# Kernel optimization log

Hardware: AMD Instinct MI355X
Metric: run time of the kernel (lower is better)

The kernel has to match this reference:

```python
import jax, jax.numpy as jnp
import numpy as np

BATCH, LENGTH = 4, 512
D_MODEL, D_STATE, EXPAND = 128, 256, 2
D_INNER = EXPAND * D_MODEL  # 256 (== D_STATE, required by the original broadcasting)


def setup_inputs() -> dict:
    key = jax.random.key(0)
    ks = jax.random.split(key, 8)
    x = jax.random.normal(ks[0], (BATCH, LENGTH, D_MODEL), jnp.float32)
    # bias-free Dense kernels, fan-in scaled; W_delta and A kept small so
    # exp(delta*A)^L stays numerically tame over L=512 steps.
    W_in = jax.random.normal(ks[1], (D_MODEL, 2 * D_INNER), jnp.float32) / np.float32(np.sqrt(D_MODEL))
    W_delta = jax.random.normal(ks[2], (D_INNER, D_INNER), jnp.float32) * np.float32(0.005)
    W_B = jax.random.normal(ks[3], (D_INNER, D_STATE), jnp.float32) / np.float32(np.sqrt(D_INNER))
    W_C = jax.random.normal(ks[4], (D_INNER, D_INNER), jnp.float32) / np.float32(np.sqrt(D_INNER))
    W_out = jax.random.normal(ks[5], (D_INNER, D_MODEL), jnp.float32) / np.float32(np.sqrt(D_INNER))
    A = jax.random.normal(ks[6], (D_INNER, D_STATE), jnp.float32) * np.float32(0.02)
    D = jnp.ones((D_INNER,), jnp.float32)  # unused by the original scan, kept for faithfulness
    return dict(x=x, W_in=W_in, W_delta=W_delta, W_B=W_B, W_C=W_C, W_out=W_out, A=A, D=D)


def reference(x, W_in, W_delta, W_B, W_C, W_out, A, D):
    # in_proj + split
    x_proj = x @ W_in                      # (b, l, 2*d_inner)
    xs, z = jnp.split(x_proj, 2, axis=-1)  # each (b, l, d_inner)
    delta = xs @ W_delta                   # (b, l, d_inner)
    Bv = xs @ W_B                          # (b, l, d_state)
    Cv = xs @ W_C                          # (b, l, d_inner)

    # discretized transition/input, exactly as the original einsums
    deltaA = jnp.exp(jnp.einsum('bld,dn->bldn', delta, A))   # (b, l, d_inner, d_state)
    deltaB = jnp.einsum('bld,bln->bldn', delta, Bv)          # (b, l, d_inner, d_state)

    def step(state, inp):
        dA_i, dB_i, x_i, C_i = inp
        # state: (b, d_inner, d_state); x broadcast over the middle axis as in tf.expand_dims(x,1)
        state = dA_i * state + dB_i * x_i[:, None, :]
        y = jnp.einsum('bdn,bn->bd', state, C_i)
        return state, y

    init = jnp.zeros((x.shape[0], D_INNER, D_STATE), xs.dtype)
    inps = (
        jnp.moveaxis(deltaA, 1, 0),  # (l, b, d, n)
        jnp.moveaxis(deltaB, 1, 0),
        jnp.moveaxis(xs, 1, 0),      # (l, b, d)
        jnp.moveaxis(Cv, 1, 0),
    )
    _, ys = jax.lax.scan(step, init, inps)   # ys: (l, b, d_inner)
    y = jnp.moveaxis(ys, 0, 1)               # (b, l, d_inner)

    y = y * jax.nn.silu(z)
    return y @ W_out                          # (b, l, d_model)
```

## Files before the change

### kernel.cpp

```cpp
#include <hip/hip_runtime.h>
#include <hip/hip_bf16.h>


#define MROWS 2048
#define DM 128
#define DI 256
#define DS 256
#define LLEN 512
#define LC 64
#define NC 8

#define LOG2E 1.44269504088896340736f

typedef short bf16x8 __attribute__((ext_vector_type(8)));
typedef float f32x4  __attribute__((ext_vector_type(4)));

__device__ __forceinline__ short f2bf(float f) {
    union { float f; unsigned u; } v; v.f = f;
    unsigned r = v.u + 0x7FFFu + ((v.u >> 16) & 1u);
    return (short)(r >> 16);
}

#define TEXP(c1, c2, c3, dl) fmaf(fmaf(fmaf((c3), (dl), (c2)), (dl), (c1)), (dl), 1.f)

__device__ __forceinline__ void tconv(float (*tile)[33],
                                      const float* __restrict__ src,
                                      short* __restrict__ dst,
                                      int Ms, int Ns, int ti, int tj, int tid)
{
    const int r = tid >> 5, c = tid & 31;
#pragma unroll
    for (int i = 0; i < 4; ++i)
        tile[r + 8 * i][c] = src[(size_t)(ti * 32 + r + 8 * i) * Ns + tj * 32 + c];
    __syncthreads();
#pragma unroll
    for (int i = 0; i < 4; ++i)
        dst[(size_t)(tj * 32 + r + 8 * i) * Ms + ti * 32 + c] = f2bf(tile[c][r + 8 * i]);
}

__global__ __launch_bounds__(256) void k_prep(
    const float* __restrict__ x, const float* __restrict__ W_in,
    const float* __restrict__ Wd, const float* __restrict__ Wb,
    const float* __restrict__ Wc, const float* __restrict__ W_out,
    short* __restrict__ x_bf, short* __restrict__ W_inT,
    short* __restrict__ WdbcT, short* __restrict__ W_outT)
{
    __shared__ float tile[32][33];
    const int bid = blockIdx.x;
    const int t = threadIdx.x;
    if (bid < 128) {
        const size_t base = (size_t)bid * 2048 + (size_t)t * 8;
        float4 f0 = *(const float4*)(x + base);
        float4 f1 = *(const float4*)(x + base + 4);
        bf16x8 o;
        o[0] = f2bf(f0.x); o[1] = f2bf(f0.y); o[2] = f2bf(f0.z); o[3] = f2bf(f0.w);
        o[4] = f2bf(f1.x); o[5] = f2bf(f1.y); o[6] = f2bf(f1.z); o[7] = f2bf(f1.w);
        *(bf16x8*)(x_bf + base) = o;
    } else if (bid < 192) {
        const int bb = bid - 128;
        tconv(tile, W_in, W_inT, 128, 512, bb & 3, bb >> 2, t);
    } else if (bid < 256) {
        const int bb = bid - 192;
        tconv(tile, Wd, WdbcT, 256, 256, bb & 7, bb >> 3, t);
    } else if (bid < 320) {
        const int bb = bid - 256;
        tconv(tile, Wb, WdbcT + (size_t)256 * 256, 256, 256, bb & 7, bb >> 3, t);
    } else if (bid < 384) {
        const int bb = bid - 320;
        tconv(tile, Wc, WdbcT + (size_t)512 * 256, 256, 256, bb & 7, bb >> 3, t);
    } else {
        const int bb = bid - 384;
        tconv(tile, W_out, W_outT, 256, 128, bb & 7, bb >> 3, t);
    }
}

#define BKK 64
#define LP  72

__device__ __forceinline__ void mfma_core64(
    const short* __restrict__ Abf, int lda,
    const short* __restrict__ BbfT, int ldb,
    int K, int r0, int n0,
    short (*As)[LP], short (*Bs)[LP], f32x4 acc[4])
{
    const int tid  = threadIdx.x;
    const int w    = tid >> 6, lane = tid & 63;
    const int srow = tid >> 2, sseg = tid & 3;
    const int frow = lane & 15, fk = (lane >> 4) << 3;

    for (int k0 = 0; k0 < K; k0 += BKK) {
        const short* ag = Abf  + (size_t)(r0 + srow) * lda + k0 + sseg * 16;
        const short* bg = BbfT + (size_t)(n0 + srow) * ldb + k0 + sseg * 16;
        bf16x8 a0 = *(const bf16x8*)ag;
        bf16x8 a1 = *(const bf16x8*)(ag + 8);
        bf16x8 b0 = *(const bf16x8*)bg;
        bf16x8 b1 = *(const bf16x8*)(bg + 8);
        __syncthreads();
        *(bf16x8*)&As[srow][sseg * 16]     = a0;
        *(bf16x8*)&As[srow][sseg * 16 + 8] = a1;
        *(bf16x8*)&Bs[srow][sseg * 16]     = b0;
        *(bf16x8*)&Bs[srow][sseg * 16 + 8] = b1;
        __syncthreads();
#pragma unroll
        for (int kk = 0; kk < BKK; kk += 32) {
            bf16x8 af = *(const bf16x8*)&As[w * 16 + frow][kk + fk];
#pragma unroll
            for (int ct = 0; ct < 4; ++ct) {
                bf16x8 bfr = *(const bf16x8*)&Bs[ct * 16 + frow][kk + fk];
                acc[ct] = __builtin_amdgcn_mfma_f32_16x16x32_bf16(af, bfr, acc[ct], 0, 0, 0);
            }
        }
    }
}

__global__ __launch_bounds__(256) void k_proj_mfma(
    const short* __restrict__ x_bf, const short* __restrict__ W_inT,
    float* __restrict__ xs, short* __restrict__ xs_bf, float* __restrict__ sz)
{
    __shared__ short As[64][LP], Bs[64][LP];
    f32x4 acc[4] = {};
    const int r0 = blockIdx.y * 64, n0 = blockIdx.x * 64;
    mfma_core64(x_bf, DM, W_inT, DM, DM, r0, n0, As, Bs, acc);
    const int lane = threadIdx.x & 63, w = threadIdx.x >> 6;
    const int rr = r0 + w * 16 + (lane >> 4) * 4;
    const int c0 = n0 + (lane & 15);
#pragma unroll
    for (int ct = 0; ct < 4; ++ct) {
        const int c = c0 + ct * 16;
#pragma unroll
        for (int rg = 0; rg < 4; ++rg) {
            const float v = acc[ct][rg];
            const int r = rr + rg;
            if (c < DI) {
                xs[(size_t)r * DI + c]    = v;
                xs_bf[(size_t)r * DI + c] = f2bf(v);
            } else {
                sz[(size_t)r * DI + (c - DI)] = v / (1.f + __expf(-v));
            }
        }
    }
}

__global__ __launch_bounds__(256) void k_dbc_mfma(
    const short* __restrict__ xs_bf, const short* __restrict__ WdbcT,
    const float* __restrict__ xs,
    float* __restrict__ dlt, float* __restrict__ u, float* __restrict__ cvv)
{
    __shared__ short As[64][LP], Bs[64][LP];
    f32x4 acc[4] = {};
    const int r0 = blockIdx.y * 64, n0 = blockIdx.x * 64;
    mfma_core64(xs_bf, DI, WdbcT, DI, DI, r0, n0, As, Bs, acc);
    const int lane = threadIdx.x & 63, w = threadIdx.x >> 6;
    const int rr = r0 + w * 16 + (lane >> 4) * 4;
    const int wsel = n0 >> 8;
    const int nb = n0 & 255;
#pragma unroll
    for (int ct = 0; ct < 4; ++ct) {
        const int c = nb + ct * 16 + (lane & 15);
#pragma unroll
        for (int rg = 0; rg < 4; ++rg) {
            const float v = acc[ct][rg];
            const size_t idx = (size_t)(rr + rg) * DI + c;
            if (wsel == 0)      dlt[idx] = v;
            else if (wsel == 1) u[idx]   = v * xs[idx];
            else                cvv[idx] = v;
        }
    }
}

__global__ __launch_bounds__(256) void k_scan1(
    const float* __restrict__ dlt, const float* __restrict__ u,
    const float* __restrict__ A,
    float* __restrict__ tc, float* __restrict__ dsum)
{
    const int lane = threadIdx.x & 63;
    const int w    = threadIdx.x >> 6;
    const int blk  = blockIdx.x;
    const int b  = blk & 3;
    const int c  = (blk >> 2) & 7;
    const int d0 = ((blk >> 5) * 4 + w) * 4;

    __shared__ float dls[4][4][LC];

    const size_t base = (size_t)b * LLEN * DI + (size_t)c * LC * DI;

    float4 dv = *(const float4*)(dlt + base + (size_t)lane * DI + d0);
    dls[w][0][lane] = dv.x;
    dls[w][1][lane] = dv.y;
    dls[w][2][lane] = dv.z;
    dls[w][3][lane] = dv.w;
    float dsv[4] = { dv.x, dv.y, dv.z, dv.w };
#pragma unroll
    for (int dd = 0; dd < 4; ++dd) {
#pragma unroll
        for (int off = 32; off > 0; off >>= 1)
            dsv[dd] += __shfl_xor(dsv[dd], off);
    }
    __syncthreads();

    float4 c1[4], c2[4], c3[4];
#pragma unroll
    for (int dd = 0; dd < 4; ++dd) {
        float4 a = *(const float4*)(A + (size_t)(d0 + dd) * DS + lane * 4);
        c1[dd] = a;
        c2[dd] = make_float4(0.5f * a.x * a.x, 0.5f * a.y * a.y,
                             0.5f * a.z * a.z, 0.5f * a.w * a.w);
        c3[dd] = make_float4(c2[dd].x * a.x * (1.f / 3.f), c2[dd].y * a.y * (1.f / 3.f),
                             c2[dd].z * a.z * (1.f / 3.f), c2[dd].w * a.w * (1.f / 3.f));
    }

    const float4* up = (const float4*)(u + base) + lane;
    float4 s[4] = {};
    float4 ub[2][4];

#define S1_PRE(NXT, G1)                                                       \
    {                                                                         \
        _Pragma("unroll")                                                     \
        for (int i = 0; i < 4; ++i)                                           \
            ub[NXT][i] = up[(size_t)((G1) * 4 + i) * 64];                     \
    }

#define S1_STEP4(CUR, G)                                                      \
    {                                                                         \
        _Pragma("unroll")                                                     \
        for (int i0 = 0; i0 < 4; ++i0) {                                      \
            const int l = (G) * 4 + i0;                                       \
            const float4 uv = ub[CUR][i0];                                    \
            _Pragma("unroll")                                                 \
            for (int dd = 0; dd < 4; ++dd) {                                  \
                const float dl = dls[w][dd][l];                               \
                s[dd].x = fmaf(TEXP(c1[dd].x, c2[dd].x, c3[dd].x, dl), s[dd].x, dl * uv.x); \
                s[dd].y = fmaf(TEXP(c1[dd].y, c2[dd].y, c3[dd].y, dl), s[dd].y, dl * uv.y); \
                s[dd].z = fmaf(TEXP(c1[dd].z, c2[dd].z, c3[dd].z, dl), s[dd].z, dl * uv.z); \
                s[dd].w = fmaf(TEXP(c1[dd].w, c2[dd].w, c3[dd].w, dl), s[dd].w, dl * uv.w); \
            }                                                                 \
        }                                                                     \
    }

    S1_PRE(0, 0)
    for (int g2 = 0; g2 < 8; ++g2) {
        S1_PRE(1, g2 * 2 + 1)
        S1_STEP4(0, g2 * 2)
        if (g2 < 7) S1_PRE(0, g2 * 2 + 2)
        S1_STEP4(1, g2 * 2 + 1)
    }
#undef S1_PRE
#undef S1_STEP4

    const size_t rbb = ((size_t)(b * 256 + d0)) * NC + c;
#pragma unroll
    for (int dd = 0; dd < 4; ++dd) {
        *(float4*)(tc + (rbb + (size_t)dd * NC) * 256 + lane * 4) = s[dd];
        if (lane == 0) dsum[rbb + dd * NC] = dsv[dd];
    }
}

__global__ __launch_bounds__(256) void k_scan2(
    const float* __restrict__ A, float* __restrict__ tc,
    const float* __restrict__ dsum)
{
    const int lane = threadIdx.x & 63;
    const int w    = threadIdx.x >> 6;
    const int blk  = blockIdx.x;
    const int b = blk & 3;
    const int d = (blk >> 2) * 4 + w;

    float4 a4 = *(const float4*)(A + (size_t)d * DS + lane * 4);
    a4.x *= LOG2E; a4.y *= LOG2E; a4.z *= LOG2E; a4.w *= LOG2E;

    const size_t rb = ((size_t)(b * 256 + d)) * NC;
    float4 s = make_float4(0.f, 0.f, 0.f, 0.f);
#pragma unroll
    for (int c = 0; c < NC; ++c) {
        float* p = tc + (rb + c) * 256 + lane * 4;
        float4 T = *(const float4*)p;
        float  Dc = dsum[rb + c];
        *(float4*)p = s;
        s.x = exp2f(a4.x * Dc) * s.x + T.x;
        s.y = exp2f(a4.y * Dc) * s.y + T.y;
        s.z = exp2f(a4.z * Dc) * s.z + T.z;
        s.w = exp2f(a4.w * Dc) * s.w + T.w;
    }
}

__global__ __launch_bounds__(256) void k_scan3(
    const float* __restrict__ dlt, const float* __restrict__ u,
    const float* __restrict__ cv, const float* __restrict__ A,
    const float* __restrict__ tc, float* __restrict__ y)
{
    const int lane = threadIdx.x & 63;
    const int w    = threadIdx.x >> 6;
    const int blk  = blockIdx.x;
    const int b  = blk & 3;
    const int c  = (blk >> 2) & 7;
    const int d0 = ((blk >> 5) * 4 + w) * 4;

    __shared__ float dls[4][4][LC];
    __shared__ float T[4][LC][33];

    const size_t base = (size_t)b * LLEN * DI + (size_t)c * LC * DI;

    float4 dv = *(const float4*)(dlt + base + (size_t)lane * DI + d0);
    dls[w][0][lane] = dv.x;
    dls[w][1][lane] = dv.y;
    dls[w][2][lane] = dv.z;
    dls[w][3][lane] = dv.w;
    __syncthreads();

    float4 c1[4], c2[4], c3[4];
#pragma unroll
    for (int dd = 0; dd < 4; ++dd) {
        float4 a = *(const float4*)(A + (size_t)(d0 + dd) * DS + lane * 4);
        c1[dd] = a;
        c2[dd] = make_float4(0.5f * a.x * a.x, 0.5f * a.y * a.y,
                             0.5f * a.z * a.z, 0.5f * a.w * a.w);
        c3[dd] = make_float4(c2[dd].x * a.x * (1.f / 3.f), c2[dd].y * a.y * (1.f / 3.f),
                             c2[dd].z * a.z * (1.f / 3.f), c2[dd].w * a.w * (1.f / 3.f));
    }

    const float4* up = (const float4*)(u + base) + lane;
    const float4* cp = (const float4*)(cv + base) + lane;
    float* yb = y + base;

    const size_t rbb = ((size_t)(b * 256 + d0)) * NC + c;
    float4 s[4];
#pragma unroll
    for (int dd = 0; dd < 4; ++dd)
        s[dd] = *(const float4*)(tc + (rbb + (size_t)dd * NC) * 256 + lane * 4);

    float4 ub[2][4], cb[2][4];
    float  p[4][8];

#define S3_PRE(NXT, G1)                                                       \
    {                                                                         \
        _Pragma("unroll")                                                     \
        for (int i = 0; i < 4; ++i) {                                         \
            ub[NXT][i] = up[(size_t)((G1) * 4 + i) * 64];                     \
            cb[NXT][i] = cp[(size_t)((G1) * 4 + i) * 64];                     \
        }                                                                     \
    }

#define S3_STEP4(CUR, G, PBASE)                                               \
    {                                                                         \
        _Pragma("unroll")                                                     \
        for (int i0 = 0; i0 < 4; ++i0) {                                      \
            const int l = (G) * 4 + i0;                                       \
            const float4 uv = ub[CUR][i0];                                    \
            const float4 cV = cb[CUR][i0];                                    \
            _Pragma("unroll")                                                 \
            for (int dd = 0; dd < 4; ++dd) {                                  \
                const float dl = dls[w][dd][l];                               \
                s[dd].x = fmaf(TEXP(c1[dd].x, c2[dd].x, c3[dd].x, dl), s[dd].x, dl * uv.x); \
                s[dd].y = fmaf(TEXP(c1[dd].y, c2[dd].y, c3[dd].y, dl), s[dd].y, dl * uv.y); \
                s[dd].z = fmaf(TEXP(c1[dd].z, c2[dd].z, c3[dd].z, dl), s[dd].z, dl * uv.z); \
                s[dd].w = fmaf(TEXP(c1[dd].w, c2[dd].w, c3[dd].w, dl), s[dd].w, dl * uv.w); \
                p[dd][(PBASE) + i0] =                                         \
                    fmaf(s[dd].w, cV.w, fmaf(s[dd].z, cV.z,                   \
                         fmaf(s[dd].y, cV.y, s[dd].x * cV.x)));               \
            }                                                                 \
        }                                                                     \
    }

#define S3_FLUSH(GODD)                                                        \
    {                                                                         \
        float* tr = &T[w][lane][0];                                           \
        _Pragma("unroll")                                                     \
        for (int dd = 0; dd < 4; ++dd) {                                      \
            *(float4*)(tr + dd * 8)     = make_float4(p[dd][0], p[dd][1], p[dd][2], p[dd][3]); \
            *(float4*)(tr + dd * 8 + 4) = make_float4(p[dd][4], p[dd][5], p[dd][6], p[dd][7]); \
        }                                                                     \
        const int cc = lane & 31, seg = lane >> 5;                            \
        float sm = 0.f;                                                       \
        _Pragma("unroll")                                                     \
        for (int r = 0; r < 32; ++r)                                          \
            sm += T[w][seg * 32 + r][cc];                                     \
        sm += __shfl_xor(sm, 32);                                             \
        if (lane < 32)                                                        \
            yb[(size_t)(((GODD) - 1) * 4 + (cc & 7)) * DI + d0 + (cc >> 3)] = sm; \
    }

    S3_PRE(0, 0)
    for (int g2 = 0; g2 < 8; ++g2) {
        S3_PRE(1, g2 * 2 + 1)
        S3_STEP4(0, g2 * 2, 0)
        if (g2 < 7) S3_PRE(0, g2 * 2 + 2)
        S3_STEP4(1, g2 * 2 + 1, 4)
        S3_FLUSH(g2 * 2 + 1)
        if ((g2 & 1) == 1) __syncthreads();
    }
#undef S3_PRE
#undef S3_STEP4
#undef S3_FLUSH
}

__global__ __launch_bounds__(256) void k_out_mfma(
    const float* __restrict__ y, const float* __restrict__ szp,
    const short* __restrict__ W_outT, float* __restrict__ out)
{
    __shared__ short As[64][LP], Bs[64][LP];
    f32x4 acc[4] = {};
    const int tid  = threadIdx.x;
    const int w    = tid >> 6, lane = tid & 63;
    const int srow = tid >> 2, sseg = tid & 3;
    const int frow = lane & 15, fk = (lane >> 4) << 3;
    const int r0 = blockIdx.y * 64, n0 = blockIdx.x * 64;

    for (int k0 = 0; k0 < DI; k0 += BKK) {
        const size_t aoff = (size_t)(r0 + srow) * DI + k0 + sseg * 16;
        float4 y0 = *(const float4*)(y + aoff);
        float4 y1 = *(const float4*)(y + aoff + 4);
        float4 y2 = *(const float4*)(y + aoff + 8);
        float4 y3 = *(const float4*)(y + aoff + 12);
        float4 s0 = *(const float4*)(szp + aoff);
        float4 s1 = *(const float4*)(szp + aoff + 4);
        float4 s2 = *(const float4*)(szp + aoff + 8);
        float4 s3 = *(const float4*)(szp + aoff + 12);
        const short* bg = W_outT + (size_t)(n0 + srow) * DI + k0 + sseg * 16;
        bf16x8 b0 = *(const bf16x8*)bg;
        bf16x8 b1 = *(const bf16x8*)(bg + 8);
        bf16x8 a0, a1;
        a0[0] = f2bf(y0.x * s0.x); a0[1] = f2bf(y0.y * s0.y);
        a0[2] = f2bf(y0.z * s0.z); a0[3] = f2bf(y0.w * s0.w);
        a0[4] = f2bf(y1.x * s1.x); a0[5] = f2bf(y1.y * s1.y);
        a0[6] = f2bf(y1.z * s1.z); a0[7] = f2bf(y1.w * s1.w);
        a1[0] = f2bf(y2.x * s2.x); a1[1] = f2bf(y2.y * s2.y);
        a1[2] = f2bf(y2.z * s2.z); a1[3] = f2bf(y2.w * s2.w);
        a1[4] = f2bf(y3.x * s3.x); a1[5] = f2bf(y3.y * s3.y);
        a1[6] = f2bf(y3.z * s3.z); a1[7] = f2bf(y3.w * s3.w);
        __syncthreads();
        *(bf16x8*)&As[srow][sseg * 16]     = a0;
        *(bf16x8*)&As[srow][sseg * 16 + 8] = a1;
        *(bf16x8*)&Bs[srow][sseg * 16]     = b0;
        *(bf16x8*)&Bs[srow][sseg * 16 + 8] = b1;
        __syncthreads();
#pragma unroll
        for (int kk = 0; kk < BKK; kk += 32) {
            bf16x8 af = *(const bf16x8*)&As[w * 16 + frow][kk + fk];
#pragma unroll
            for (int ct = 0; ct < 4; ++ct) {
                bf16x8 bfr = *(const bf16x8*)&Bs[ct * 16 + frow][kk + fk];
                acc[ct] = __builtin_amdgcn_mfma_f32_16x16x32_bf16(af, bfr, acc[ct], 0, 0, 0);
            }
        }
    }

    const int rr = r0 + w * 16 + (lane >> 4) * 4;
    const int c0 = n0 + (lane & 15);
#pragma unroll
    for (int ct = 0; ct < 4; ++ct) {
        const int c = c0 + ct * 16;
#pragma unroll
        for (int rg = 0; rg < 4; ++rg)
            out[(size_t)(rr + rg) * DM + c] = acc[ct][rg];
    }
}

extern "C" void kernel_launch(void* const* d_in, const int* in_sizes, int n_in,
                              void* d_out, int out_size, void* d_ws, size_t ws_size,
                              hipStream_t stream)
{
    const float* x       = (const float*)d_in[0];
    const float* W_in    = (const float*)d_in[1];
    const float* W_delta = (const float*)d_in[2];
    const float* W_B     = (const float*)d_in[3];
    const float* W_C     = (const float*)d_in[4];
    const float* W_out   = (const float*)d_in[5];
    const float* A       = (const float*)d_in[6];

    float* out = (float*)d_out;
    float* ws  = (float*)d_ws;

    const size_t S = (size_t)MROWS * DI;
    float* xs  = ws;
    float* sz  = ws + S;
    float* dlt = ws + 2 * S;
    float* u   = ws + 3 * S;
    float* cv  = ws + 4 * S;
    float* yv  = ws + 5 * S;
    float* tc  = ws + 6 * S;
    float* dsm = ws + 6 * S + (size_t)1024 * NC * 256;

    short* bfb    = (short*)(dsm + 1024 * NC);
    short* x_bf   = bfb;
    short* xs_bf  = x_bf + (size_t)MROWS * DM;
    short* W_inT  = xs_bf + (size_t)MROWS * DI;
    short* WdbcT  = W_inT + (size_t)512 * DM;
    short* W_outT = WdbcT + (size_t)768 * DI;

    k_prep     <<<dim3(416), 256, 0, stream>>>(x, W_in, W_delta, W_B, W_C, W_out,
                                               x_bf, W_inT, WdbcT, W_outT);
    k_proj_mfma<<<dim3(8, 32), 256, 0, stream>>>(x_bf, W_inT, xs, xs_bf, sz);
    k_dbc_mfma <<<dim3(12, 32), 256, 0, stream>>>(xs_bf, WdbcT, xs, dlt, u, cv);
    k_scan1    <<<dim3(512), 256, 0, stream>>>(dlt, u, A, tc, dsm);
    k_scan2    <<<dim3(256), 256, 0, stream>>>(A, tc, dsm);
    k_scan3    <<<dim3(512), 256, 0, stream>>>(dlt, u, cv, A, tc, yv);
    k_out_mfma <<<dim3(2, 32), 256, 0, stream>>>(yv, sz, W_outT, out);
}
```

Measured before the change: 76.54 us.

## Fuse prep into projection GEMM, halve scan chunk length, simplify scan loops

Folds the bf16 conversion and weight-transpose prep kernel into the input projection kernel, which now converts x and W_in on the fly and uses extra blocks to transpose the other weights. This removes one launch and the x_bf/W_inT round trip. The scan chunk length drops from 64 to 32 with 16 chunks, doubling the scan1/scan3 grids for more parallelism at the cost of a longer inter-chunk scan2, which now preloads its chunk values into registers. The scan loops drop their double-buffered prefetch and some __syncthreads, and add launch-bounds occupancy hints.

Result: no change. 77.77 us (+1.6%).

```diff
diff --git a/kernel.cpp b/kernel.cpp
--- a/kernel.cpp
+++ b/kernel.cpp
@@ -7,8 +7,8 @@
 #define DI 256
 #define DS 256
 #define LLEN 512
-#define LC 64
-#define NC 8
+#define LC 32
+#define NC 16
 
 #define LOG2E 1.44269504088896340736f
 
@@ -38,39 +38,84 @@
         dst[(size_t)(tj * 32 + r + 8 * i) * Ms + ti * 32 + c] = f2bf(tile[c][r + 8 * i]);
 }
 
-__global__ __launch_bounds__(256) void k_prep(
+__global__ __launch_bounds__(256) void k_proj_mfma(
     const float* __restrict__ x, const float* __restrict__ W_in,
     const float* __restrict__ Wd, const float* __restrict__ Wb,
     const float* __restrict__ Wc, const float* __restrict__ W_out,
-    short* __restrict__ x_bf, short* __restrict__ W_inT,
+    float* __restrict__ xs, short* __restrict__ xs_bf, float* __restrict__ sz,
     short* __restrict__ WdbcT, short* __restrict__ W_outT)
 {
-    __shared__ float tile[32][33];
-    const int bid = blockIdx.x;
     const int t = threadIdx.x;
-    if (bid < 128) {
-        const size_t base = (size_t)bid * 2048 + (size_t)t * 8;
-        float4 f0 = *(const float4*)(x + base);
-        float4 f1 = *(const float4*)(x + base + 4);
-        bf16x8 o;
-        o[0] = f2bf(f0.x); o[1] = f2bf(f0.y); o[2] = f2bf(f0.z); o[3] = f2bf(f0.w);
-        o[4] = f2bf(f1.x); o[5] = f2bf(f1.y); o[6] = f2bf(f1.z); o[7] = f2bf(f1.w);
-        *(bf16x8*)(x_bf + base) = o;
-    } else if (bid < 192) {
-        const int bb = bid - 128;
-        tconv(tile, W_in, W_inT, 128, 512, bb & 3, bb >> 2, t);
-    } else if (bid < 256) {
-        const int bb = bid - 192;
-        tconv(tile, Wd, WdbcT, 256, 256, bb & 7, bb >> 3, t);
-    } else if (bid < 320) {
-        const int bb = bid - 256;
-        tconv(tile, Wb, WdbcT + (size_t)256 * 256, 256, 256, bb & 7, bb >> 3, t);
-    } else if (bid < 384) {
-        const int bb = bid - 320;
-        tconv(tile, Wc, WdbcT + (size_t)512 * 256, 256, 256, bb & 7, bb >> 3, t);
-    } else {
-        const int bb = bid - 384;
-        tconv(tile, W_out, W_outT, 256, 128, bb & 7, bb >> 3, t);
+
+    if (blockIdx.x >= 8) {
+        __shared__ float tile[32][33];
+        const int uu = (blockIdx.x - 8) * 32 + blockIdx.y;
+        if (uu < 64)       tconv(tile, Wd,    WdbcT,                       256, 256, uu & 7,         uu >> 3,         t);
+        else if (uu < 128) tconv(tile, Wb,    WdbcT + (size_t)256 * 256,   256, 256, (uu - 64) & 7,  (uu - 64) >> 3,  t);
+        else if (uu < 192) tconv(tile, Wc,    WdbcT + (size_t)512 * 256,   256, 256, (uu - 128) & 7, (uu - 128) >> 3, t);
+        else if (uu < 224) tconv(tile, W_out, W_outT,                      256, 128, (uu - 192) & 7, (uu - 192) >> 3, t);
+        return;
+    }
+
+    __shared__ short As[64][136];
+    __shared__ short Bs[64][136];
+    f32x4 acc[4] = {};
+    const int w = t >> 6, lane = t & 63;
+    const int srow = t >> 2, sseg = t & 3;
+    const int frow = lane & 15, fk = (lane >> 4) << 3;
+    const int r0 = blockIdx.y * 64, n0 = blockIdx.x * 64;
+
+    {
+        const float* ap = x + (size_t)(r0 + srow) * DM + sseg * 32;
+        short tmp[32];
+#pragma unroll
+        for (int j = 0; j < 8; ++j) {
+            float4 f = *(const float4*)(ap + j * 4);
+            tmp[j * 4 + 0] = f2bf(f.x); tmp[j * 4 + 1] = f2bf(f.y);
+            tmp[j * 4 + 2] = f2bf(f.z); tmp[j * 4 + 3] = f2bf(f.w);
+        }
+#pragma unroll
+        for (int m = 0; m < 4; ++m)
+            *(bf16x8*)&As[srow][sseg * 32 + m * 8] = *(bf16x8*)&tmp[m * 8];
+    }
+    {
+#pragma unroll
+        for (int i = 0; i < 32; i += 2) {
+            const int k = sseg * 32 + i;
+            float f0 = W_in[(size_t)k * 512 + n0 + srow];
+            float f1 = W_in[(size_t)(k + 1) * 512 + n0 + srow];
+            unsigned pk = (unsigned short)f2bf(f0) | ((unsigned)(unsigned short)f2bf(f1) << 16);
+            *(unsigned*)&Bs[srow][k] = pk;
+        }
+    }
+    __syncthreads();
+
+#pragma unroll
+    for (int kk = 0; kk < 128; kk += 32) {
+        bf16x8 af = *(const bf16x8*)&As[w * 16 + frow][kk + fk];
+#pragma unroll
+        for (int ct = 0; ct < 4; ++ct) {
+            bf16x8 bfr = *(const bf16x8*)&Bs[ct * 16 + frow][kk + fk];
+            acc[ct] = __builtin_amdgcn_mfma_f32_16x16x32_bf16(af, bfr, acc[ct], 0, 0, 0);
+        }
+    }
+
+    const int rr = r0 + w * 16 + (lane >> 4) * 4;
+    const int c0 = n0 + (lane & 15);
+#pragma unroll
+    for (int ct = 0; ct < 4; ++ct) {
+        const int c = c0 + ct * 16;
+#pragma unroll
+        for (int rg = 0; rg < 4; ++rg) {
+            const float v = acc[ct][rg];
+            const int r = rr + rg;
+            if (c < DI) {
+                xs[(size_t)r * DI + c]    = v;
+                xs_bf[(size_t)r * DI + c] = f2bf(v);
+            } else {
+                sz[(size_t)r * DI + (c - DI)] = v / (1.f + __expf(-v));
+            }
+        }
     }
 }
 
@@ -113,34 +158,6 @@
     }
 }
 
-__global__ __launch_bounds__(256) void k_proj_mfma(
-    const short* __restrict__ x_bf, const short* __restrict__ W_inT,
-    float* __restrict__ xs, short* __restrict__ xs_bf, float* __restrict__ sz)
-{
-    __shared__ short As[64][LP], Bs[64][LP];
-    f32x4 acc[4] = {};
-    const int r0 = blockIdx.y * 64, n0 = blockIdx.x * 64;
-    mfma_core64(x_bf, DM, W_inT, DM, DM, r0, n0, As, Bs, acc);
-    const int lane = threadIdx.x & 63, w = threadIdx.x >> 6;
-    const int rr = r0 + w * 16 + (lane >> 4) * 4;
-    const int c0 = n0 + (lane & 15);
-#pragma unroll
-    for (int ct = 0; ct < 4; ++ct) {
-        const int c = c0 + ct * 16;
-#pragma unroll
-        for (int rg = 0; rg < 4; ++rg) {
-            const float v = acc[ct][rg];
-            const int r = rr + rg;
-            if (c < DI) {
-                xs[(size_t)r * DI + c]    = v;
-                xs_bf[(size_t)r * DI + c] = f2bf(v);
-            } else {
-                sz[(size_t)r * DI + (c - DI)] = v / (1.f + __expf(-v));
-            }
-        }
-    }
-}
-
 __global__ __launch_bounds__(256) void k_dbc_mfma(
     const short* __restrict__ xs_bf, const short* __restrict__ WdbcT,
     const float* __restrict__ xs,
@@ -168,7 +185,8 @@
     }
 }
 
-__global__ __launch_bounds__(256) void k_scan1(
+
+__global__ __launch_bounds__(256, 4) void k_scan1(
     const float* __restrict__ dlt, const float* __restrict__ u,
     const float* __restrict__ A,
     float* __restrict__ tc, float* __restrict__ dsum)
@@ -177,18 +195,21 @@
     const int w    = threadIdx.x >> 6;
     const int blk  = blockIdx.x;
     const int b  = blk & 3;
-    const int c  = (blk >> 2) & 7;
-    const int d0 = ((blk >> 5) * 4 + w) * 4;
+    const int c  = (blk >> 2) & 15;
+    const int d0 = ((blk >> 6) * 4 + w) * 4;
 
     __shared__ float dls[4][4][LC];
 
     const size_t base = (size_t)b * LLEN * DI + (size_t)c * LC * DI;
 
-    float4 dv = *(const float4*)(dlt + base + (size_t)lane * DI + d0);
-    dls[w][0][lane] = dv.x;
-    dls[w][1][lane] = dv.y;
-    dls[w][2][lane] = dv.z;
-    dls[w][3][lane] = dv.w;
+    float4 dv = make_float4(0.f, 0.f, 0.f, 0.f);
+    if (lane < LC) {
+        dv = *(const float4*)(dlt + base + (size_t)lane * DI + d0);
+        dls[w][0][lane] = dv.x;
+        dls[w][1][lane] = dv.y;
+        dls[w][2][lane] = dv.z;
+        dls[w][3][lane] = dv.w;
+    }
     float dsv[4] = { dv.x, dv.y, dv.z, dv.w };
 #pragma unroll
     for (int dd = 0; dd < 4; ++dd) {
@@ -196,7 +217,6 @@
         for (int off = 32; off > 0; off >>= 1)
             dsv[dd] += __shfl_xor(dsv[dd], off);
     }
-    __syncthreads();
 
     float4 c1[4], c2[4], c3[4];
 #pragma unroll
@@ -211,41 +231,25 @@
 
     const float4* up = (const float4*)(u + base) + lane;
     float4 s[4] = {};
-    float4 ub[2][4];
-
-#define S1_PRE(NXT, G1)                                                       \
-    {                                                                         \
-        _Pragma("unroll")                                                     \
-        for (int i = 0; i < 4; ++i)                                           \
-            ub[NXT][i] = up[(size_t)((G1) * 4 + i) * 64];                     \
-    }
-
-#define S1_STEP4(CUR, G)                                                      \
-    {                                                                         \
-        _Pragma("unroll")                                                     \
-        for (int i0 = 0; i0 < 4; ++i0) {                                      \
-            const int l = (G) * 4 + i0;                                       \
-            const float4 uv = ub[CUR][i0];                                    \
-            _Pragma("unroll")                                                 \
-            for (int dd = 0; dd < 4; ++dd) {                                  \
-                const float dl = dls[w][dd][l];                               \
-                s[dd].x = fmaf(TEXP(c1[dd].x, c2[dd].x, c3[dd].x, dl), s[dd].x, dl * uv.x); \
-                s[dd].y = fmaf(TEXP(c1[dd].y, c2[dd].y, c3[dd].y, dl), s[dd].y, dl * uv.y); \
-                s[dd].z = fmaf(TEXP(c1[dd].z, c2[dd].z, c3[dd].z, dl), s[dd].z, dl * uv.z); \
-                s[dd].w = fmaf(TEXP(c1[dd].w, c2[dd].w, c3[dd].w, dl), s[dd].w, dl * uv.w); \
-            }                                                                 \
-        }                                                                     \
-    }
-
-    S1_PRE(0, 0)
-    for (int g2 = 0; g2 < 8; ++g2) {
-        S1_PRE(1, g2 * 2 + 1)
-        S1_STEP4(0, g2 * 2)
-        if (g2 < 7) S1_PRE(0, g2 * 2 + 2)
-        S1_STEP4(1, g2 * 2 + 1)
-    }
-#undef S1_PRE
-#undef S1_STEP4
+
+    for (int g = 0; g < LC / 4; ++g) {
+        float4 uv[4];
+#pragma unroll
+        for (int i = 0; i < 4; ++i)
+            uv[i] = up[(size_t)(g * 4 + i) * 64];
+#pragma unroll
+        for (int i = 0; i < 4; ++i) {
+            const int l = g * 4 + i;
+#pragma unroll
+            for (int dd = 0; dd < 4; ++dd) {
+                const float dl = dls[w][dd][l];
+                s[dd].x = fmaf(TEXP(c1[dd].x, c2[dd].x, c3[dd].x, dl), s[dd].x, dl * uv[i].x);
+                s[dd].y = fmaf(TEXP(c1[dd].y, c2[dd].y, c3[dd].y, dl), s[dd].y, dl * uv[i].y);
+                s[dd].z = fmaf(TEXP(c1[dd].z, c2[dd].z, c3[dd].z, dl), s[dd].z, dl * uv[i].z);
+                s[dd].w = fmaf(TEXP(c1[dd].w, c2[dd].w, c3[dd].w, dl), s[dd].w, dl * uv[i].w);
+            }
+        }
+    }
 
     const size_t rbb = ((size_t)(b * 256 + d0)) * NC + c;
 #pragma unroll
@@ -269,21 +273,29 @@
     a4.x *= LOG2E; a4.y *= LOG2E; a4.z *= LOG2E; a4.w *= LOG2E;
 
     const size_t rb = ((size_t)(b * 256 + d)) * NC;
+    float4 T[NC];
+    float  Dc[NC];
+#pragma unroll
+    for (int c = 0; c < NC; ++c) {
+        T[c]  = *(const float4*)(tc + (rb + c) * 256 + lane * 4);
+        Dc[c] = dsum[rb + c];
+    }
     float4 s = make_float4(0.f, 0.f, 0.f, 0.f);
 #pragma unroll
     for (int c = 0; c < NC; ++c) {
-        float* p = tc + (rb + c) * 256 + lane * 4;
-        float4 T = *(const float4*)p;
-        float  Dc = dsum[rb + c];
-        *(float4*)p = s;
-        s.x = exp2f(a4.x * Dc) * s.x + T.x;
-        s.y = exp2f(a4.y * Dc) * s.y + T.y;
-        s.z = exp2f(a4.z * Dc) * s.z + T.z;
-        s.w = exp2f(a4.w * Dc) * s.w + T.w;
-    }
-}
-
-__global__ __launch_bounds__(256) void k_scan3(
+        float4 tmp = T[c];
+        T[c] = s;
+        s.x = exp2f(a4.x * Dc[c]) * s.x + tmp.x;
+        s.y = exp2f(a4.y * Dc[c]) * s.y + tmp.y;
+        s.z = exp2f(a4.z * Dc[c]) * s.z + tmp.z;
+        s.w = exp2f(a4.w * Dc[c]) * s.w + tmp.w;
+    }
+#pragma unroll
+    for (int c = 0; c < NC; ++c)
+        *(float4*)(tc + (rb + c) * 256 + lane * 4) = T[c];
+}
+
+__global__ __launch_bounds__(256, 4) void k_scan3(
     const float* __restrict__ dlt, const float* __restrict__ u,
     const float* __restrict__ cv, const float* __restrict__ A,
     const float* __restrict__ tc, float* __restrict__ y)
@@ -292,20 +304,21 @@
     const int w    = threadIdx.x >> 6;
     const int blk  = blockIdx.x;
     const int b  = blk & 3;
-    const int c  = (blk >> 2) & 7;
-    const int d0 = ((blk >> 5) * 4 + w) * 4;
+    const int c  = (blk >> 2) & 15;
+    const int d0 = ((blk >> 6) * 4 + w) * 4;
 
     __shared__ float dls[4][4][LC];
-    __shared__ float T[4][LC][33];
+    __shared__ float T[4][64][33];
 
     const size_t base = (size_t)b * LLEN * DI + (size_t)c * LC * DI;
 
-    float4 dv = *(const float4*)(dlt + base + (size_t)lane * DI + d0);
-    dls[w][0][lane] = dv.x;
-    dls[w][1][lane] = dv.y;
-    dls[w][2][lane] = dv.z;
-    dls[w][3][lane] = dv.w;
-    __syncthreads();
+    if (lane < LC) {
+        float4 dv = *(const float4*)(dlt + base + (size_t)lane * DI + d0);
+        dls[w][0][lane] = dv.x;
+        dls[w][1][lane] = dv.y;
+        dls[w][2][lane] = dv.z;
+        dls[w][3][lane] = dv.w;
+    }
 
     float4 c1[4], c2[4], c3[4];
 #pragma unroll
@@ -328,69 +341,41 @@
     for (int dd = 0; dd < 4; ++dd)
         s[dd] = *(const float4*)(tc + (rbb + (size_t)dd * NC) * 256 + lane * 4);
 
-    float4 ub[2][4], cb[2][4];
-    float  p[4][8];
-
-#define S3_PRE(NXT, G1)                                                       \
-    {                                                                         \
-        _Pragma("unroll")                                                     \
-        for (int i = 0; i < 4; ++i) {                                         \
-            ub[NXT][i] = up[(size_t)((G1) * 4 + i) * 64];                     \
-            cb[NXT][i] = cp[(size_t)((G1) * 4 + i) * 64];                     \
-        }                                                                     \
-    }
-
-#define S3_STEP4(CUR, G, PBASE)                                               \
-    {                                                                         \
-        _Pragma("unroll")                                                     \
-        for (int i0 = 0; i0 < 4; ++i0) {                                      \
-            const int l = (G) * 4 + i0;                                       \
-            const float4 uv = ub[CUR][i0];                                    \
-            const float4 cV = cb[CUR][i0];                                    \
-            _Pragma("unroll")                                                 \
-            for (int dd = 0; dd < 4; ++dd) {                                  \
-                const float dl = dls[w][dd][l];                               \
-                s[dd].x = fmaf(TEXP(c1[dd].x, c2[dd].x, c3[dd].x, dl), s[dd].x, dl * uv.x); \
-                s[dd].y = fmaf(TEXP(c1[dd].y, c2[dd].y, c3[dd].y, dl), s[dd].y, dl * uv.y); \
-                s[dd].z = fmaf(TEXP(c1[dd].z, c2[dd].z, c3[dd].z, dl), s[dd].z, dl * uv.z); \
-                s[dd].w = fmaf(TEXP(c1[dd].w, c2[dd].w, c3[dd].w, dl), s[dd].w, dl * uv.w); \
-                p[dd][(PBASE) + i0] =                                         \
-                    fmaf(s[dd].w, cV.w, fmaf(s[dd].z, cV.z,                   \
-                         fmaf(s[dd].y, cV.y, s[dd].x * cV.x)));               \
-            }                                                                 \
-        }                                                                     \
-    }
-
-#define S3_FLUSH(GODD)                                                        \
-    {                                                                         \
-        float* tr = &T[w][lane][0];                                           \
-        _Pragma("unroll")                                                     \
-        for (int dd = 0; dd < 4; ++dd) {                                      \
-            *(float4*)(tr + dd * 8)     = make_float4(p[dd][0], p[dd][1], p[dd][2], p[dd][3]); \
-            *(float4*)(tr + dd * 8 + 4) = make_float4(p[dd][4], p[dd][5], p[dd][6], p[dd][7]); \
-        }                                                                     \
-        const int cc = lane & 31, seg = lane >> 5;                            \
-        float sm = 0.f;                                                       \
-        _Pragma("unroll")                                                     \
-        for (int r = 0; r < 32; ++r)                                          \
-            sm += T[w][seg * 32 + r][cc];                                     \
-        sm += __shfl_xor(sm, 32);                                             \
-        if (lane < 32)                                                        \
-            yb[(size_t)(((GODD) - 1) * 4 + (cc & 7)) * DI + d0 + (cc >> 3)] = sm; \
-    }
-
-    S3_PRE(0, 0)
-    for (int g2 = 0; g2 < 8; ++g2) {
-        S3_PRE(1, g2 * 2 + 1)
-        S3_STEP4(0, g2 * 2, 0)
-        if (g2 < 7) S3_PRE(0, g2 * 2 + 2)
-        S3_STEP4(1, g2 * 2 + 1, 4)
-        S3_FLUSH(g2 * 2 + 1)
-        if ((g2 & 1) == 1) __syncthreads();
-    }
-#undef S3_PRE
-#undef S3_STEP4
-#undef S3_FLUSH
+    const int cc = lane & 31, seg = lane >> 5;
+
+    for (int g = 0; g < LC / 4; ++g) {
+        float4 uv[4], cV[4];
+#pragma unroll
+        for (int i = 0; i < 4; ++i) {
+            uv[i] = up[(size_t)(g * 4 + i) * 64];
+            cV[i] = cp[(size_t)(g * 4 + i) * 64];
+        }
+#pragma unroll
+        for (int i = 0; i < 4; ++i) {
+            const int l = g * 4 + i;
+            const int lc = l & 7;
+#pragma unroll
+            for (int dd = 0; dd < 4; ++dd) {
+                const float dl = dls[w][dd][l];
+                s[dd].x = fmaf(TEXP(c1[dd].x, c2[dd].x, c3[dd].x, dl), s[dd].x, dl * uv[i].x);
+                s[dd].y = fmaf(TEXP(c1[dd].y, c2[dd].y, c3[dd].y, dl), s[dd].y, dl * uv[i].y);
+                s[dd].z = fmaf(TEXP(c1[dd].z, c2[dd].z, c3[dd].z, dl), s[dd].z, dl * uv[i].z);
+                s[dd].w = fmaf(TEXP(c1[dd].w, c2[dd].w, c3[dd].w, dl), s[dd].w, dl * uv[i].w);
+                T[w][lane][dd * 8 + lc] =
+                    fmaf(s[dd].w, cV[i].w, fmaf(s[dd].z, cV[i].z,
+                         fmaf(s[dd].y, cV[i].y, s[dd].x * cV[i].x)));
+            }
+        }
+        if (g & 1) {
+            float sm = 0.f;
+#pragma unroll
+            for (int r = 0; r < 32; ++r)
+                sm += T[w][seg * 32 + r][cc];
+            sm += __shfl_xor(sm, 32);
+            if (lane < 32)
+                yb[(size_t)((g >> 1) * 8 + (cc & 7)) * DI + d0 + (cc >> 3)] = sm;
+        }
+    }
 }
 
 __global__ __launch_bounds__(256) void k_out_mfma(
@@ -478,21 +463,17 @@
     float* cv  = ws + 4 * S;
     float* yv  = ws + 5 * S;
     float* tc  = ws + 6 * S;
-    float* dsm = ws + 6 * S + (size_t)1024 * NC * 256;
-
-    short* bfb    = (short*)(dsm + 1024 * NC);
-    short* x_bf   = bfb;
-    short* xs_bf  = x_bf + (size_t)MROWS * DM;
-    short* W_inT  = xs_bf + (size_t)MROWS * DI;
-    short* WdbcT  = W_inT + (size_t)512 * DM;
+    float* dsm = tc + (size_t)1024 * NC * 256;
+
+    short* xs_bf  = (short*)(dsm + (size_t)1024 * NC);
+    short* WdbcT  = xs_bf + (size_t)MROWS * DI;
     short* W_outT = WdbcT + (size_t)768 * DI;
 
-    k_prep     <<<dim3(416), 256, 0, stream>>>(x, W_in, W_delta, W_B, W_C, W_out,
-                                               x_bf, W_inT, WdbcT, W_outT);
-    k_proj_mfma<<<dim3(8, 32), 256, 0, stream>>>(x_bf, W_inT, xs, xs_bf, sz);
+    k_proj_mfma<<<dim3(15, 32), 256, 0, stream>>>(x, W_in, W_delta, W_B, W_C, W_out,
+                                                  xs, xs_bf, sz, WdbcT, W_outT);
     k_dbc_mfma <<<dim3(12, 32), 256, 0, stream>>>(xs_bf, WdbcT, xs, dlt, u, cv);
-    k_scan1    <<<dim3(512), 256, 0, stream>>>(dlt, u, A, tc, dsm);
+    k_scan1    <<<dim3(1024), 256, 0, stream>>>(dlt, u, A, tc, dsm);
     k_scan2    <<<dim3(256), 256, 0, stream>>>(A, tc, dsm);
-    k_scan3    <<<dim3(512), 256, 0, stream>>>(dlt, u, cv, A, tc, yv);
+    k_scan3    <<<dim3(1024), 256, 0, stream>>>(dlt, u, cv, A, tc, yv);
     k_out_mfma <<<dim3(2, 32), 256, 0, stream>>>(yv, sz, W_outT, out);
 }
```
